# Kernel tuning notes

Hardware: AMD Instinct MI355X
Metric: run time of the kernel (lower is better)

Reference implementation:

```python
import jax, jax.numpy as jnp
import numpy as np

N, E, F, B, S, T, D = 50000, 150000, 100000, 64, 32, 32, 3
RADIUS = 1.0
SCALE = 500.0


def setup_inputs() -> dict:
    key = jax.random.key(0)
    ks = jax.random.split(key, 8)
    x = jax.random.normal(ks[0], (N, D), dtype=jnp.float32)
    node_weights = jax.random.uniform(ks[1], (N,), dtype=jnp.float32)
    edge_index = jax.random.randint(ks[2], (2, E), 0, N)
    edge_weights = jax.random.uniform(ks[3], (E,), dtype=jnp.float32)
    face = jax.random.randint(ks[4], (3, F), 0, N)
    face_weights = jax.random.uniform(ks[5], (F,), dtype=jnp.float32)
    batch = jnp.sort(jax.random.randint(ks[6], (N,), 0, B))
    v = jax.random.normal(ks[7], (D, T), dtype=jnp.float32)
    v = v / jnp.linalg.norm(v, axis=0, keepdims=True)  # unit directions
    lin = jnp.linspace(-RADIUS, RADIUS, S, dtype=jnp.float32)
    return {"x": x, "node_weights": node_weights, "edge_index": edge_index,
            "edge_weights": edge_weights, "face": face, "face_weights": face_weights,
            "batch": batch, "v": v, "lin": lin}


def compute_ecc(h, index, lin, num_segments):
    # h: [M, T] simplex heights; lin: [S] thresholds
    # sigmoid bump at each threshold, then scatter-add per graph -> [B, S, T]
    ecc = jax.nn.sigmoid(SCALE * (lin[None, :, None] - h[:, None, :]))  # [M, S, T]
    return jax.ops.segment_sum(ecc, index, num_segments=num_segments)


def reference(x, node_weights, edge_index, edge_weights, face, face_weights, batch, v, lin):
    nh = (x * node_weights[:, None]) @ v                      # [N, T] node heights
    eh = jnp.max(nh[edge_index], axis=0) * edge_weights[:, None]  # [E, T]
    fh = jnp.max(nh[face], axis=0) * face_weights[:, None]        # [F, T]
    idx_e = batch[edge_index[0]]
    idx_f = batch[face[0]]
    ect = (compute_ecc(nh, batch, lin, B)
           - compute_ecc(eh, idx_e, lin, B)
           + compute_ecc(fh, idx_f, lin, B))                  # [B, S, T]
    return ect  # normalized=False -> squeeze() is a no-op here
```

## Files before the change

### kernel.cpp

```cpp
#include <hip/hip_runtime.h>
#include <hip/hip_bf16.h>

#define N_NODES 50000
#define N_EDGES 150000
#define N_FACES 100000
#define NB 64
#define NS 32
#define NT 32
#define SCALE_C 500.0f
#define DLIN (2.0f / 31.0f)
#define INV_DLIN (31.0f / 2.0f)
#define WIN 0.02f
#define DSZ (NB * NS * NT)
#define CH 256
#define WG 4

__device__ __forceinline__ float sigf(float z) {
    float e = __expf(-z);
    return __builtin_amdgcn_rcpf(1.0f + e);
}

__global__ void nh_kernel(const float* __restrict__ x, const float* __restrict__ nw,
                          const float* __restrict__ v, float* __restrict__ nh) {
    int idx = blockIdx.x * blockDim.x + threadIdx.x;
    if (idx >= N_NODES * NT) return;
    int n = idx >> 5, t = idx & 31;
    float w = nw[n];
    float x0 = x[3 * n], x1 = x[3 * n + 1], x2 = x[3 * n + 2];
    nh[idx] = w * (x0 * v[t] + x1 * v[NT + t] + x2 * v[2 * NT + t]);
}

__global__ void hist_kernel(const int* __restrict__ ei, const int* __restrict__ fi,
                            const int* __restrict__ batch,
                            int* __restrict__ ge, int* __restrict__ gf,
                            int* __restrict__ hist_e, int* __restrict__ hist_f) {
    __shared__ int he[NB], hf[NB];
    if (threadIdx.x < NB) { he[threadIdx.x] = 0; hf[threadIdx.x] = 0; }
    __syncthreads();
    int stride = gridDim.x * blockDim.x;
    for (int i = blockIdx.x * blockDim.x + threadIdx.x; i < N_EDGES; i += stride) {
        int g = batch[ei[i]];
        ge[i] = g;
        atomicAdd(&he[g], 1);
    }
    for (int i = blockIdx.x * blockDim.x + threadIdx.x; i < N_FACES; i += stride) {
        int g = batch[fi[i]];
        gf[i] = g;
        atomicAdd(&hf[g], 1);
    }
    __syncthreads();
    if (threadIdx.x < NB) {
        if (he[threadIdx.x]) atomicAdd(&hist_e[threadIdx.x], he[threadIdx.x]);
        if (hf[threadIdx.x]) atomicAdd(&hist_f[threadIdx.x], hf[threadIdx.x]);
    }
}

__global__ void scan_kernel(const int* __restrict__ hist_e, const int* __restrict__ hist_f,
                            int* __restrict__ cur_e, int* __restrict__ cur_f) {
    __shared__ int sh[128];
    int tid = threadIdx.x;
    sh[tid] = (tid < 64) ? hist_e[tid] : hist_f[tid - 64];
    __syncthreads();
    int which = tid >> 6, lane = tid & 63;
    int s = 0;
    for (int g = 0; g < lane; g++) s += sh[which * 64 + g];
    if (which == 0) cur_e[lane] = s; else cur_f[lane] = s;
}

__global__ void scatter_kernel(const int* __restrict__ garr, int M,
                               int* __restrict__ cursors,
                               int* __restrict__ perm, int* __restrict__ gs) {
    __shared__ int cnt[NB], base[NB];
    int c0 = blockIdx.x * 1024;
    if (threadIdx.x < NB) cnt[threadIdx.x] = 0;
    __syncthreads();
    int gv[4], ev[4], n = 0;
    #pragma unroll
    for (int k = 0; k < 4; k++) {
        int i = c0 + k * 256 + threadIdx.x;
        if (i < M) { ev[n] = i; gv[n] = garr[i]; atomicAdd(&cnt[gv[n]], 1); n++; }
    }
    __syncthreads();
    if (threadIdx.x < NB) {
        base[threadIdx.x] = atomicAdd(&cursors[threadIdx.x], cnt[threadIdx.x]);
        cnt[threadIdx.x] = 0;
    }
    __syncthreads();
    for (int k = 0; k < n; k++) {
        int pos = base[gv[k]] + atomicAdd(&cnt[gv[k]], 1);
        perm[pos] = ev[k];
        gs[pos] = gv[k];
    }
}

__global__ __launch_bounds__(256) void accum_kernel(
    const float* __restrict__ nh, const int* __restrict__ batch,
    const int* __restrict__ ei, const float* __restrict__ ew,
    const int* __restrict__ perm_e, const int* __restrict__ gs_e,
    const int* __restrict__ fi, const float* __restrict__ fw,
    const int* __restrict__ perm_f, const int* __restrict__ gs_f,
    float* __restrict__ delta, int nbn, int nbe)
{
    __shared__ float tile[WG * NS * NT];
    int t = threadIdx.x & 31, slot = threadIdx.x >> 5;
    int bid = blockIdx.x;
    int type, i0, i1;
    float sign;
    if (bid < nbn) {
        type = 0; i0 = bid * CH; i1 = min(i0 + CH, N_NODES); sign = 1.0f;
    } else if (bid < nbn + nbe) {
        type = 1; int b = bid - nbn; i0 = b * CH; i1 = min(i0 + CH, N_EDGES); sign = -1.0f;
    } else {
        type = 2; int b = bid - nbn - nbe; i0 = b * CH; i1 = min(i0 + CH, N_FACES); sign = 1.0f;
    }
    int g0 = (type == 0) ? batch[i0] : (type == 1 ? gs_e[i0] : gs_f[i0]);

    for (int k = threadIdx.x; k < WG * NS * NT; k += 256) tile[k] = 0.0f;
    __syncthreads();

    #define EMIT(S, VAL) do { \
        int _o = (S) * NT + t; \
        if (wi < WG) atomicAdd(&tile[wi * (NS * NT) + _o], (VAL)); \
        else atomicAdd(&delta[g * (NS * NT) + _o], sign * (VAL)); } while (0)

    for (int i = i0 + slot; i < i1; i += 8) {
        float h;
        int g;
        if (type == 0) {
            g = batch[i];
            h = nh[i * NT + t];
        } else if (type == 1) {
            g = gs_e[i];
            int e = perm_e[i];
            int na = ei[e], nb = ei[N_EDGES + e];
            h = fmaxf(nh[na * NT + t], nh[nb * NT + t]) * ew[e];
        } else {
            g = gs_f[i];
            int f = perm_f[i];
            int na = fi[f], nb = fi[N_FACES + f], nc = fi[2 * N_FACES + f];
            h = fmaxf(fmaxf(nh[na * NT + t], nh[nb * NT + t]), nh[nc * NT + t]) * fw[f];
        }
        int wi = g - g0;
        int slo_u = (int)ceilf((h - WIN + 1.0f) * INV_DLIN);
        int shi_u = (int)floorf((h + WIN + 1.0f) * INV_DLIN);
        int slo = slo_u < 0 ? 0 : slo_u;
        int shi = shi_u > (NS - 1) ? (NS - 1) : shi_u;
        float prev = 0.0f;
        for (int s = slo; s <= shi; s++) {
            float vs = sigf(SCALE_C * (-1.0f + s * DLIN - h));
            EMIT(s, vs - prev);
            prev = vs;
        }
        int sstep = shi_u + 1;
        if (sstep <= NS - 1) {
            int sc = sstep < 0 ? 0 : sstep;
            EMIT(sc, 1.0f - prev);
        }
    }
    #undef EMIT

    __syncthreads();
    for (int k = threadIdx.x; k < WG * NS * NT; k += 256) {
        float vv = tile[k];
        if (vv != 0.0f) {
            int wi = k >> 10, cell = k & (NS * NT - 1);
            int g = g0 + wi;
            if (g < NB) atomicAdd(&delta[g * (NS * NT) + cell], sign * vv);
        }
    }
}

__global__ void finalize_kernel(const float* __restrict__ delta, float* __restrict__ out) {
    int idx = blockIdx.x * blockDim.x + threadIdx.x;
    if (idx >= NB * NT) return;
    int g = idx >> 5, t = idx & 31;
    const float* dg = delta + (g * NS) * NT + t;
    float* og = out + (g * NS) * NT + t;
    float run = 0.0f;
    for (int s = 0; s < NS; s++) {
        run += dg[s * NT];
        og[s * NT] = run;
    }
}

extern "C" void kernel_launch(void* const* d_in, const int* in_sizes, int n_in,
                              void* d_out, int out_size, void* d_ws, size_t ws_size,
                              hipStream_t stream) {
    const float* x     = (const float*)d_in[0];
    const float* nw    = (const float*)d_in[1];
    const int*   ei    = (const int*)d_in[2];
    const float* ew    = (const float*)d_in[3];
    const int*   fi    = (const int*)d_in[4];
    const float* fw    = (const float*)d_in[5];
    const int*   batch = (const int*)d_in[6];
    const float* v     = (const float*)d_in[7];
    const float* lin   = (const float*)d_in[8];
    (void)lin; (void)in_sizes; (void)n_in; (void)ws_size;
    float* out = (float*)d_out;

    char* ws = (char*)d_ws;
    float* delta  = (float*)ws;
    int*   hist_e = (int*)(ws + DSZ * 4);
    int*   hist_f = hist_e + 64;
    int*   cur_e  = hist_e + 128;
    int*   cur_f  = hist_e + 192;
    float* nh     = (float*)(ws + DSZ * 4 + 1024);
    int*   ge     = (int*)((char*)nh + (size_t)N_NODES * NT * 4);
    int*   gf     = ge + N_EDGES;
    int*   perm_e = gf + N_FACES;
    int*   gs_e   = perm_e + N_EDGES;
    int*   perm_f = gs_e + N_EDGES;
    int*   gs_f   = perm_f + N_FACES;

    hipMemsetAsync(delta, 0, DSZ * 4 + 1024, stream);

    nh_kernel<<<(N_NODES * NT + 255) / 256, 256, 0, stream>>>(x, nw, v, nh);
    hist_kernel<<<512, 256, 0, stream>>>(ei, fi, batch, ge, gf, hist_e, hist_f);
    scan_kernel<<<1, 128, 0, stream>>>(hist_e, hist_f, cur_e, cur_f);
    scatter_kernel<<<(N_EDGES + 1023) / 1024, 256, 0, stream>>>(ge, N_EDGES, cur_e, perm_e, gs_e);
    scatter_kernel<<<(N_FACES + 1023) / 1024, 256, 0, stream>>>(gf, N_FACES, cur_f, perm_f, gs_f);

    int nbn = (N_NODES + CH - 1) / CH;
    int nbe = (N_EDGES + CH - 1) / CH;
    int nbf = (N_FACES + CH - 1) / CH;
    accum_kernel<<<nbn + nbe + nbf, 256, 0, stream>>>(
        nh, batch, ei, ew, perm_e, gs_e, fi, fw, perm_f, gs_f, delta, nbn, nbe);
    finalize_kernel<<<(NB * NT + 255) / 256, 256, 0, stream>>>(delta, out);
}
```

Before: 197.8 us.

## Fuse prep kernels, scatter sorted edge/face payloads, halve accumulation chunk size

```diff
diff --git a/kernel.cpp b/kernel.cpp
--- a/kernel.cpp
+++ b/kernel.cpp
@@ -12,7 +12,7 @@
 #define INV_DLIN (31.0f / 2.0f)
 #define WIN 0.02f
 #define DSZ (NB * NS * NT)
-#define CH 256
+#define CH 128
 #define WG 4
 
 __device__ __forceinline__ float sigf(float z) {
@@ -20,34 +20,31 @@
     return __builtin_amdgcn_rcpf(1.0f + e);
 }
 
-__global__ void nh_kernel(const float* __restrict__ x, const float* __restrict__ nw,
-                          const float* __restrict__ v, float* __restrict__ nh) {
-    int idx = blockIdx.x * blockDim.x + threadIdx.x;
-    if (idx >= N_NODES * NT) return;
-    int n = idx >> 5, t = idx & 31;
-    float w = nw[n];
-    float x0 = x[3 * n], x1 = x[3 * n + 1], x2 = x[3 * n + 2];
-    nh[idx] = w * (x0 * v[t] + x1 * v[NT + t] + x2 * v[2 * NT + t]);
-}
-
-__global__ void hist_kernel(const int* __restrict__ ei, const int* __restrict__ fi,
-                            const int* __restrict__ batch,
-                            int* __restrict__ ge, int* __restrict__ gf,
-                            int* __restrict__ hist_e, int* __restrict__ hist_f) {
+__global__ __launch_bounds__(256) void prep_kernel(
+    const float* __restrict__ x, const float* __restrict__ nw,
+    const float* __restrict__ v, const int* __restrict__ ei,
+    const int* __restrict__ fi, const int* __restrict__ batch,
+    float* __restrict__ nh, int* __restrict__ hist_e, int* __restrict__ hist_f,
+    int nhB)
+{
+    if (blockIdx.x < nhB) {
+        int idx = blockIdx.x * 256 + threadIdx.x;
+        if (idx < N_NODES * NT) {
+            int n = idx >> 5, t = idx & 31;
+            float w = nw[n];
+            nh[idx] = w * (x[3 * n] * v[t] + x[3 * n + 1] * v[NT + t] + x[3 * n + 2] * v[2 * NT + t]);
+        }
+        return;
+    }
     __shared__ int he[NB], hf[NB];
     if (threadIdx.x < NB) { he[threadIdx.x] = 0; hf[threadIdx.x] = 0; }
     __syncthreads();
-    int stride = gridDim.x * blockDim.x;
-    for (int i = blockIdx.x * blockDim.x + threadIdx.x; i < N_EDGES; i += stride) {
-        int g = batch[ei[i]];
-        ge[i] = g;
-        atomicAdd(&he[g], 1);
-    }
-    for (int i = blockIdx.x * blockDim.x + threadIdx.x; i < N_FACES; i += stride) {
-        int g = batch[fi[i]];
-        gf[i] = g;
-        atomicAdd(&hf[g], 1);
-    }
+    int b = blockIdx.x - nhB;
+    int stride = (gridDim.x - nhB) * 256;
+    for (int i = b * 256 + threadIdx.x; i < N_EDGES; i += stride)
+        atomicAdd(&he[batch[ei[i]]], 1);
+    for (int i = b * 256 + threadIdx.x; i < N_FACES; i += stride)
+        atomicAdd(&hf[batch[fi[i]]], 1);
     __syncthreads();
     if (threadIdx.x < NB) {
         if (he[threadIdx.x]) atomicAdd(&hist_e[threadIdx.x], he[threadIdx.x]);
@@ -67,38 +64,53 @@
     if (which == 0) cur_e[lane] = s; else cur_f[lane] = s;
 }
 
-__global__ void scatter_kernel(const int* __restrict__ garr, int M,
-                               int* __restrict__ cursors,
-                               int* __restrict__ perm, int* __restrict__ gs) {
+__global__ __launch_bounds__(256) void scatter_kernel(
+    const int* __restrict__ ei, const float* __restrict__ ew,
+    const int* __restrict__ fi, const float* __restrict__ fw,
+    const int* __restrict__ batch, int* __restrict__ cur_e, int* __restrict__ cur_f,
+    int* __restrict__ gs_e, int* __restrict__ ea, int* __restrict__ eb, float* __restrict__ ews,
+    int* __restrict__ gs_f, int* __restrict__ fa, int* __restrict__ fb,
+    int* __restrict__ fc, float* __restrict__ fws, int nbE)
+{
     __shared__ int cnt[NB], base[NB];
-    int c0 = blockIdx.x * 1024;
+    bool isE = blockIdx.x < nbE;
+    int bb = isE ? blockIdx.x : blockIdx.x - nbE;
+    int M = isE ? N_EDGES : N_FACES;
+    const int* idx0 = isE ? ei : fi;
+    int c0 = bb * 1024;
     if (threadIdx.x < NB) cnt[threadIdx.x] = 0;
     __syncthreads();
-    int gv[4], ev[4], n = 0;
+    int gv[4], iv[4], n = 0;
     #pragma unroll
     for (int k = 0; k < 4; k++) {
         int i = c0 + k * 256 + threadIdx.x;
-        if (i < M) { ev[n] = i; gv[n] = garr[i]; atomicAdd(&cnt[gv[n]], 1); n++; }
+        if (i < M) { iv[n] = i; gv[n] = batch[idx0[i]]; atomicAdd(&cnt[gv[n]], 1); n++; }
     }
     __syncthreads();
     if (threadIdx.x < NB) {
-        base[threadIdx.x] = atomicAdd(&cursors[threadIdx.x], cnt[threadIdx.x]);
+        base[threadIdx.x] = atomicAdd((isE ? cur_e : cur_f) + threadIdx.x, cnt[threadIdx.x]);
         cnt[threadIdx.x] = 0;
     }
     __syncthreads();
     for (int k = 0; k < n; k++) {
-        int pos = base[gv[k]] + atomicAdd(&cnt[gv[k]], 1);
-        perm[pos] = ev[k];
-        gs[pos] = gv[k];
+        int g = gv[k], i = iv[k];
+        int pos = base[g] + atomicAdd(&cnt[g], 1);
+        if (isE) {
+            gs_e[pos] = g; ea[pos] = ei[i]; eb[pos] = ei[N_EDGES + i]; ews[pos] = ew[i];
+        } else {
+            gs_f[pos] = g; fa[pos] = fi[i]; fb[pos] = fi[N_FACES + i];
+            fc[pos] = fi[2 * N_FACES + i]; fws[pos] = fw[i];
+        }
     }
 }
 
 __global__ __launch_bounds__(256) void accum_kernel(
     const float* __restrict__ nh, const int* __restrict__ batch,
-    const int* __restrict__ ei, const float* __restrict__ ew,
-    const int* __restrict__ perm_e, const int* __restrict__ gs_e,
-    const int* __restrict__ fi, const float* __restrict__ fw,
-    const int* __restrict__ perm_f, const int* __restrict__ gs_f,
+    const int* __restrict__ gs_e, const int* __restrict__ ea,
+    const int* __restrict__ eb, const float* __restrict__ ews,
+    const int* __restrict__ gs_f, const int* __restrict__ fa,
+    const int* __restrict__ fb, const int* __restrict__ fc,
+    const float* __restrict__ fws,
     float* __restrict__ delta, int nbn, int nbe)
 {
     __shared__ float tile[WG * NS * NT];
@@ -131,14 +143,12 @@
             h = nh[i * NT + t];
         } else if (type == 1) {
             g = gs_e[i];
-            int e = perm_e[i];
-            int na = ei[e], nb = ei[N_EDGES + e];
-            h = fmaxf(nh[na * NT + t], nh[nb * NT + t]) * ew[e];
+            int na = ea[i], nb2 = eb[i];
+            h = fmaxf(nh[na * NT + t], nh[nb2 * NT + t]) * ews[i];
         } else {
             g = gs_f[i];
-            int f = perm_f[i];
-            int na = fi[f], nb = fi[N_FACES + f], nc = fi[2 * N_FACES + f];
-            h = fmaxf(fmaxf(nh[na * NT + t], nh[nb * NT + t]), nh[nc * NT + t]) * fw[f];
+            int na = fa[i], nb2 = fb[i], nc = fc[i];
+            h = fmaxf(fmaxf(nh[na * NT + t], nh[nb2 * NT + t]), nh[nc * NT + t]) * fws[i];
         }
         int wi = g - g0;
         int slo_u = (int)ceilf((h - WIN + 1.0f) * INV_DLIN);
@@ -205,25 +215,28 @@
     int*   cur_e  = hist_e + 128;
     int*   cur_f  = hist_e + 192;
     float* nh     = (float*)(ws + DSZ * 4 + 1024);
-    int*   ge     = (int*)((char*)nh + (size_t)N_NODES * NT * 4);
-    int*   gf     = ge + N_EDGES;
-    int*   perm_e = gf + N_FACES;
-    int*   gs_e   = perm_e + N_EDGES;
-    int*   perm_f = gs_e + N_EDGES;
-    int*   gs_f   = perm_f + N_FACES;
+    int*   gs_e   = (int*)((char*)nh + (size_t)N_NODES * NT * 4);
+    int*   ea     = gs_e + N_EDGES;
+    int*   eb     = ea + N_EDGES;
+    float* ews    = (float*)(eb + N_EDGES);
+    int*   gs_f   = (int*)(ews + N_EDGES);
+    int*   fa     = gs_f + N_FACES;
+    int*   fb     = fa + N_FACES;
+    int*   fc     = fb + N_FACES;
+    float* fws    = (float*)(fc + N_FACES);
 
     hipMemsetAsync(delta, 0, DSZ * 4 + 1024, stream);
 
-    nh_kernel<<<(N_NODES * NT + 255) / 256, 256, 0, stream>>>(x, nw, v, nh);
-    hist_kernel<<<512, 256, 0, stream>>>(ei, fi, batch, ge, gf, hist_e, hist_f);
+    int nhB = (N_NODES * NT + 255) / 256;
+    prep_kernel<<<nhB + 512, 256, 0, stream>>>(x, nw, v, ei, fi, batch, nh, hist_e, hist_f, nhB);
     scan_kernel<<<1, 128, 0, stream>>>(hist_e, hist_f, cur_e, cur_f);
-    scatter_kernel<<<(N_EDGES + 1023) / 1024, 256, 0, stream>>>(ge, N_EDGES, cur_e, perm_e, gs_e);
-    scatter_kernel<<<(N_FACES + 1023) / 1024, 256, 0, stream>>>(gf, N_FACES, cur_f, perm_f, gs_f);
-
+    int nbE = (N_EDGES + 1023) / 1024, nbF = (N_FACES + 1023) / 1024;
+    scatter_kernel<<<nbE + nbF, 256, 0, stream>>>(ei, ew, fi, fw, batch, cur_e, cur_f,
+                                                  gs_e, ea, eb, ews, gs_f, fa, fb, fc, fws, nbE);
     int nbn = (N_NODES + CH - 1) / CH;
     int nbe = (N_EDGES + CH - 1) / CH;
     int nbf = (N_FACES + CH - 1) / CH;
     accum_kernel<<<nbn + nbe + nbf, 256, 0, stream>>>(
-        nh, batch, ei, ew, perm_e, gs_e, fi, fw, perm_f, gs_f, delta, nbn, nbe);
+        nh, batch, gs_e, ea, eb, ews, gs_f, fa, fb, fc, fws, delta, nbn, nbe);
     finalize_kernel<<<(NB * NT + 255) / 256, 256, 0, stream>>>(delta, out);
 }
```

Measured after the change: 189.9 us. -4.0%, faster.
